# Kernel tuning notes

Hardware: AMD Instinct MI355X
Metric: run time of the kernel (lower is better)

## Reference

```python
import jax, jax.numpy as jnp
import numpy as np

N = 10000      # nodes
E = 100000     # edges
C = 32         # in_channels == hidden_channels == out_channels
ED = 4         # edge_dim
G = 64         # number of graphs in the batch
EPS = 1e-5     # BatchNorm eps


def setup_inputs() -> dict:
    key = jax.random.key(0)
    ks = jax.random.split(key, 20)
    rn = lambda k, shape, s=0.05: jax.random.normal(k, shape, dtype=jnp.float32) * s
    return {
        "x": jax.random.normal(ks[0], (N, C), dtype=jnp.float32),
        "edge_attr": jax.random.normal(ks[1], (E, ED), dtype=jnp.float32),
        # edge MLP 1: ED -> C -> C*C ; NNConv1 root/bias
        "e1_w1": rn(ks[2], (ED, C)), "e1_b1": jnp.zeros((C,), jnp.float32),
        "e1_w2": rn(ks[3], (C, C * C)), "e1_b2": jnp.zeros((C * C,), jnp.float32),
        "root1": rn(ks[4], (C, C)), "bias1": jnp.zeros((C,), jnp.float32),
        # edge MLP 2: ED -> C -> C*C ; NNConv2 root/bias
        "e2_w1": rn(ks[5], (ED, C)), "e2_b1": jnp.zeros((C,), jnp.float32),
        "e2_w2": rn(ks[6], (C, C * C)), "e2_b2": jnp.zeros((C * C,), jnp.float32),
        "root2": rn(ks[7], (C, C)), "bias2": jnp.zeros((C,), jnp.float32),
        # BatchNorm (eval mode: running stats)
        "bn1_g": jnp.ones((C,), jnp.float32), "bn1_b": jnp.zeros((C,), jnp.float32),
        "bn1_m": rn(ks[8], (C,), 0.1), "bn1_v": 1.0 + 0.1 * jax.random.uniform(ks[9], (C,), dtype=jnp.float32),
        "bn2_g": jnp.ones((C,), jnp.float32), "bn2_b": jnp.zeros((C,), jnp.float32),
        "bn2_m": rn(ks[10], (C,), 0.1), "bn2_v": 1.0 + 0.1 * jax.random.uniform(ks[11], (C,), dtype=jnp.float32),
        # readout: C -> C//2 -> 1
        "r1_w": rn(ks[12], (C, C // 2)), "r1_b": jnp.zeros((C // 2,), jnp.float32),
        "r2_w": rn(ks[13], (C // 2, 1)), "r2_b": jnp.zeros((1,), jnp.float32),
        "edge_index": jax.random.randint(ks[14], (2, E), 0, N),
        "batch": jnp.sort(jax.random.randint(ks[15], (N,), 0, G)),
    }


def _nnconv(x, edge_index, edge_attr, w1, b1, w2, b2, root, bias):
    # edge MLP -> per-edge weight matrix [E, C, C]
    h = jax.nn.relu(edge_attr @ w1 + b1)
    W = (h @ w2 + b2).reshape(E, C, C)
    src, dst = edge_index[0], edge_index[1]
    # gather source features, per-edge matmul, scatter-mean to target nodes
    msg = jnp.einsum('ei,eio->eo', x[src], W)                      # [E, C]
    agg = jax.ops.segment_sum(msg, dst, num_segments=N)            # [N, C]
    cnt = jax.ops.segment_sum(jnp.ones((E,), x.dtype), dst, num_segments=N)
    agg = agg / jnp.maximum(cnt, 1.0)[:, None]
    return agg + x @ root + bias


def _bn(x, g, b, m, v):
    return (x - m) * jax.lax.rsqrt(v + EPS) * g + b


def reference(x, edge_attr,
              e1_w1, e1_b1, e1_w2, e1_b2, root1, bias1,
              e2_w1, e2_b1, e2_w2, e2_b2, root2, bias2,
              bn1_g, bn1_b, bn1_m, bn1_v,
              bn2_g, bn2_b, bn2_m, bn2_v,
              r1_w, r1_b, r2_w, r2_b,
              edge_index, batch):
    h = jax.nn.relu(_bn(_nnconv(x, edge_index, edge_attr, e1_w1, e1_b1, e1_w2, e1_b2, root1, bias1),
                        bn1_g, bn1_b, bn1_m, bn1_v))
    h = jax.nn.relu(_bn(_nnconv(h, edge_index, edge_attr, e2_w1, e2_b1, e2_w2, e2_b2, root2, bias2),
                        bn2_g, bn2_b, bn2_m, bn2_v))
    # global mean pool over graphs
    psum = jax.ops.segment_sum(h, batch, num_segments=G)           # [G, C]
    pcnt = jax.ops.segment_sum(jnp.ones((N,), h.dtype), batch, num_segments=G)
    pooled = psum / jnp.maximum(pcnt, 1.0)[:, None]
    # readout MLP (dropout is identity in eval)
    return jax.nn.relu(pooled @ r1_w + r1_b) @ r2_w + r2_b          # [G, 1]
```

## Files before the change

kernel.cpp:

```cpp
#include <hip/hip_runtime.h>

#define NN 10000
#define EE 100000
#define CC 32
#define GG 64
#define EPSV 1e-5f
#define NB 8
#define SLOTS 1056
#define HST 36
#define PST 36
#define PNODE (32*PST)
#define EBLK (EE/8)
#define WBLK 160

__global__ __launch_bounds__(256) void k_init(const float* __restrict__ edge_attr,
        const float* __restrict__ w1a, const float* __restrict__ b1a,
        const float* __restrict__ w1b, const float* __restrict__ b1b,
        const int* __restrict__ ei,
        float* __restrict__ hbuf1, float* __restrict__ hbuf2,
        int* __restrict__ cnt, int* __restrict__ deg,
        const float* __restrict__ w2a, const float* __restrict__ b2a,
        const float* __restrict__ w2b, const float* __restrict__ b2b,
        float* __restrict__ w2r1, float* __restrict__ w2r2) {
    int blk = blockIdx.x;
    int t = threadIdx.x;
    if (blk < EBLK) {
        int e = blk * 8 + (t >> 5);
        int o = t & 31;
        float4 a = *(const float4*)&edge_attr[(size_t)e * 4];
        float ha = fmaxf(a.x * w1a[o] + a.y * w1a[32 + o] + a.z * w1a[64 + o] + a.w * w1a[96 + o] + b1a[o], 0.f);
        float hb = fmaxf(a.x * w1b[o] + a.y * w1b[32 + o] + a.z * w1b[64 + o] + a.w * w1b[96 + o] + b1b[o], 0.f);
        hbuf1[(size_t)e * HST + o] = ha;
        hbuf2[(size_t)e * HST + o] = hb;
        if (o < 4) {
            float pad = (o == 0) ? 1.f : 0.f;
            hbuf1[(size_t)e * HST + 32 + o] = pad;
            hbuf2[(size_t)e * HST + 32 + o] = pad;
        }
        if (o == 0) {
            atomicAdd(&cnt[ei[EE + e]], 1);
            atomicAdd(&deg[ei[e]], 1);
        }
    } else {
        int b2i = blk - EBLK;
        int s = (b2i % 5) * 256 + t;
        int i = b2i / 5;
        if (s < SLOTS) {
            float va = (s < 1024) ? w2a[(s >> 5) * 1024 + i * 32 + (s & 31)]
                                  : b2a[i * 32 + (s - 1024)];
            float vb = (s < 1024) ? w2b[(s >> 5) * 1024 + i * 32 + (s & 31)]
                                  : b2b[i * 32 + (s - 1024)];
            w2r1[i * SLOTS + s] = va;
            w2r2[i * SLOTS + s] = vb;
        }
    }
}

__global__ __launch_bounds__(1024) void k_scan(const int* __restrict__ deg,
                                               int* __restrict__ rowptr,
                                               int* __restrict__ cursor) {
    __shared__ int buf[1024];
    int t = threadIdx.x;
    int v[10]; int s = 0;
    int base = t * 10;
    #pragma unroll
    for (int k = 0; k < 10; k++) {
        int idx = base + k;
        v[k] = (idx < NN) ? deg[idx] : 0;
        s += v[k];
    }
    buf[t] = s;
    for (int off = 1; off < 1024; off <<= 1) {
        __syncthreads();
        int val = buf[t] + ((t >= off) ? buf[t - off] : 0);
        __syncthreads();
        buf[t] = val;
    }
    __syncthreads();
    int carry = (t > 0) ? buf[t - 1] : 0;
    #pragma unroll
    for (int k = 0; k < 10; k++) {
        int idx = base + k;
        if (idx < NN) { rowptr[idx] = carry; cursor[idx] = carry; }
        carry += v[k];
    }
    if (t == 1023) rowptr[NN] = buf[1023];
}

__global__ void k_scatter(const int* __restrict__ ei,
                          int* __restrict__ cursor, int* __restrict__ csr_eid) {
    int e = blockIdx.x * blockDim.x + threadIdx.x;
    if (e >= EE) return;
    int pos = atomicAdd(&cursor[ei[e]], 1);
    csr_eid[pos] = e;
}

__global__ __launch_bounds__(256, 3) void k_fused3(const float* __restrict__ x,
        const float* __restrict__ hbuf,
        const float* __restrict__ w2r,
        const int* __restrict__ ei, const int* __restrict__ rowptr,
        const int* __restrict__ csr_eid, float* __restrict__ agg) {
    __shared__ float xs[NB][32];
    __shared__ float P2[NB * PNODE];
    int t = threadIdx.x;
    int o = t & 31;
    int cb = 4 * (t >> 5);
    int n0 = blockIdx.x * NB;

    xs[t >> 5][t & 31] = x[n0 * 32 + t];
    __syncthreads();

    {
        float acc[4][NB];
        #pragma unroll
        for (int k = 0; k < 4; k++)
            #pragma unroll
            for (int n = 0; n < NB; n++) acc[k][n] = 0.f;
        #pragma unroll
        for (int j = 0; j < 8; j++) {
            float wk[4][4];
            #pragma unroll
            for (int r = 0; r < 4; r++)
                #pragma unroll
                for (int k = 0; k < 4; k++)
                    wk[r][k] = w2r[(4 * j + r) * SLOTS + (cb + k) * 32 + o];
            #pragma unroll
            for (int n = 0; n < NB; n++) {
                float4 xq = *(const float4*)&xs[n][4 * j];
                #pragma unroll
                for (int k = 0; k < 4; k++)
                    acc[k][n] += xq.x * wk[0][k] + xq.y * wk[1][k]
                               + xq.z * wk[2][k] + xq.w * wk[3][k];
            }
        }
        #pragma unroll
        for (int n = 0; n < NB; n++) {
            float4 st = make_float4(acc[0][n], acc[1][n], acc[2][n], acc[3][n]);
            *(float4*)&P2[n * PNODE + o * PST + cb] = st;
        }
    }
    if (t < 32) {
        float wb[32];
        #pragma unroll
        for (int i = 0; i < 32; i++) wb[i] = w2r[i * SLOTS + 1024 + t];
        #pragma unroll
        for (int n = 0; n < NB; n++) {
            float b = 0.f;
            #pragma unroll
            for (int j = 0; j < 8; j++) {
                float4 xq = *(const float4*)&xs[n][4 * j];
                b += xq.x * wb[4 * j] + xq.y * wb[4 * j + 1]
                   + xq.z * wb[4 * j + 2] + xq.w * wb[4 * j + 3];
            }
            *(float4*)&P2[n * PNODE + t * PST + 32] = make_float4(b, 0.f, 0.f, 0.f);
        }
    }
    __syncthreads();

    int ebase = rowptr[n0];
    int eend  = rowptr[n0 + NB];
    int grp = t >> 5;
    int pos = ebase + grp;
    int e_c = 0, src_c = 0, dst_c = 0;
    float4 hq[9];
    if (pos < eend) {
        e_c = csr_eid[pos];
        src_c = ei[e_c];
        dst_c = ei[EE + e_c];
        const float* hb = &hbuf[(size_t)e_c * HST];
        #pragma unroll
        for (int b = 0; b < 9; b++) hq[b] = *(const float4*)&hb[4 * b];
    }
    while (pos < eend) {
        int pos_n = pos + 8;
        int e_n = 0, src_n = 0, dst_n = 0;
        float4 hq_n[9];
        if (pos_n < eend) {
            e_n = csr_eid[pos_n];
            src_n = ei[e_n];
            dst_n = ei[EE + e_n];
            const float* hbn = &hbuf[(size_t)e_n * HST];
            #pragma unroll
            for (int b = 0; b < 9; b++) hq_n[b] = *(const float4*)&hbn[4 * b];
        }
        const float* Pn = &P2[(src_c - n0) * PNODE + o * PST];
        float msg = 0.f;
        #pragma unroll
        for (int b = 0; b < 9; b++) {
            float4 pq = *(const float4*)&Pn[4 * b];
            msg += hq[b].x * pq.x + hq[b].y * pq.y
                 + hq[b].z * pq.z + hq[b].w * pq.w;
        }
        atomicAdd(&agg[(size_t)dst_c * 32 + o], msg);
        pos = pos_n; e_c = e_n; src_c = src_n; dst_c = dst_n;
        #pragma unroll
        for (int b = 0; b < 9; b++) hq[b] = hq_n[b];
    }
}

__global__ __launch_bounds__(256) void k_combine(const float* __restrict__ x_in,
        float* __restrict__ agg, const int* __restrict__ cnt,
        const float* __restrict__ root, const float* __restrict__ bias,
        const float* __restrict__ bng, const float* __restrict__ bnb,
        const float* __restrict__ bnm, const float* __restrict__ bnv,
        float* __restrict__ x_out, float* __restrict__ psum,
        const int* __restrict__ batch) {
    __shared__ float xs[8][32];
    __shared__ float vals[8][32];
    __shared__ int gb[8];
    int t = threadIdx.x;
    int n0 = blockIdx.x * 8;
    xs[t >> 5][t & 31] = x_in[n0 * 32 + t];
    __syncthreads();
    int k = t >> 5, o = t & 31, n = n0 + k;
    float r = bias[o];
    #pragma unroll
    for (int i = 0; i < 32; i++) r += xs[k][i] * root[i * 32 + o];
    float a = agg[(size_t)n * 32 + o] / fmaxf((float)cnt[n], 1.f);
    float val = a + r;
    val = (val - bnm[o]) * rsqrtf(bnv[o] + EPSV) * bng[o] + bnb[o];
    val = fmaxf(val, 0.f);
    if (x_out) {
        x_out[(size_t)n * 32 + o] = val;
        agg[(size_t)n * 32 + o] = 0.f;
    }
    if (psum) {
        vals[k][o] = val;
        if (o == 0) gb[k] = batch[n];
        __syncthreads();
        if (k == 0) {
            float acc = vals[0][o];
            int g = gb[0];
            #pragma unroll
            for (int k2 = 1; k2 < 8; k2++) {
                if (gb[k2] == g) acc += vals[k2][o];
                else {
                    atomicAdd(&psum[(size_t)g * 32 + o], acc);
                    g = gb[k2]; acc = vals[k2][o];
                }
            }
            atomicAdd(&psum[(size_t)g * 32 + o], acc);
        }
    }
}

__global__ __launch_bounds__(256) void k_readout(const float* __restrict__ psum,
        const int* __restrict__ batch,
        const float* __restrict__ r1w, const float* __restrict__ r1b,
        const float* __restrict__ r2w, const float* __restrict__ r2b,
        float* __restrict__ out) {
    __shared__ float w1s[32 * 16];
    __shared__ float b1s[16];
    __shared__ float w2s[16];
    __shared__ float ps[GG * 32];
    int t = threadIdx.x;
    int cnt_g = 0;
    if (t < GG) {
        int lo = 0, hi = NN;
        while (lo < hi) { int m = (lo + hi) >> 1; if (batch[m] < t) lo = m + 1; else hi = m; }
        int lb = lo;
        lo = 0; hi = NN;
        while (lo < hi) { int m = (lo + hi) >> 1; if (batch[m] < t + 1) lo = m + 1; else hi = m; }
        cnt_g = lo - lb;
    }
    w1s[t] = r1w[t];
    w1s[t + 256] = r1w[t + 256];
    if (t < 16) { b1s[t] = r1b[t]; w2s[t] = r2w[t]; }
    #pragma unroll
    for (int i = 0; i < GG * 32 / 256; i++) ps[t + i * 256] = psum[t + i * 256];
    __syncthreads();
    if (t < GG) {
        float inv = 1.f / fmaxf((float)cnt_g, 1.f);
        float acc = r2b[0];
        #pragma unroll
        for (int j = 0; j < 16; j++) {
            float dot = 0.f;
            #pragma unroll
            for (int c = 0; c < 32; c++) dot += ps[t * 32 + c] * w1s[c * 16 + j];
            float z = dot * inv + b1s[j];
            acc += fmaxf(z, 0.f) * w2s[j];
        }
        out[t] = acc;
    }
}

extern "C" void kernel_launch(void* const* d_in, const int* in_sizes, int n_in,
                              void* d_out, int out_size, void* d_ws, size_t ws_size,
                              hipStream_t stream) {
    const float* x       = (const float*)d_in[0];
    const float* eattr   = (const float*)d_in[1];
    const float* e1_w1   = (const float*)d_in[2];
    const float* e1_b1   = (const float*)d_in[3];
    const float* e1_w2   = (const float*)d_in[4];
    const float* e1_b2   = (const float*)d_in[5];
    const float* root1   = (const float*)d_in[6];
    const float* bias1   = (const float*)d_in[7];
    const float* e2_w1   = (const float*)d_in[8];
    const float* e2_b1   = (const float*)d_in[9];
    const float* e2_w2   = (const float*)d_in[10];
    const float* e2_b2   = (const float*)d_in[11];
    const float* root2   = (const float*)d_in[12];
    const float* bias2   = (const float*)d_in[13];
    const float* bn1_g   = (const float*)d_in[14];
    const float* bn1_b   = (const float*)d_in[15];
    const float* bn1_m   = (const float*)d_in[16];
    const float* bn1_v   = (const float*)d_in[17];
    const float* bn2_g   = (const float*)d_in[18];
    const float* bn2_b   = (const float*)d_in[19];
    const float* bn2_m   = (const float*)d_in[20];
    const float* bn2_v   = (const float*)d_in[21];
    const float* r1_w    = (const float*)d_in[22];
    const float* r1_b    = (const float*)d_in[23];
    const float* r2_w    = (const float*)d_in[24];
    const float* r2_b    = (const float*)d_in[25];
    const int*   ei      = (const int*)d_in[26];
    const int*   batch   = (const int*)d_in[27];

    char* ws = (char*)d_ws;
    float* hbuf1  = (float*)(ws);
    float* hbuf2  = (float*)(ws + 14400000);
    float* w2r1   = (float*)(ws + 28800000);
    float* w2r2   = (float*)(ws + 28935168);
    float* agg    = (float*)(ws + 29070336);
    int*   cnt    = (int*)  (ws + 30350336);
    int*   deg    = (int*)  (ws + 30390336);
    float* psum   = (float*)(ws + 30430336);
    float* xmid   = (float*)(ws + 30438528);
    int*   rowptr = (int*)  (ws + 31718528);
    int*   cursor = (int*)  (ws + 31758592);
    int*   csr    = (int*)  (ws + 31798592);

    hipMemsetAsync(ws + 29070336, 0, 1368192, stream);

    k_init<<<EBLK + WBLK, 256, 0, stream>>>(eattr, e1_w1, e1_b1, e2_w1, e2_b1, ei,
                                            hbuf1, hbuf2, cnt, deg,
                                            e1_w2, e1_b2, e2_w2, e2_b2, w2r1, w2r2);
    k_scan<<<1, 1024, 0, stream>>>(deg, rowptr, cursor);
    k_scatter<<<(EE + 255) / 256, 256, 0, stream>>>(ei, cursor, csr);

    k_fused3<<<NN / NB, 256, 0, stream>>>(x, hbuf1, w2r1, ei, rowptr, csr, agg);
    k_combine<<<NN / 8, 256, 0, stream>>>(x, agg, cnt, root1, bias1,
                                          bn1_g, bn1_b, bn1_m, bn1_v,
                                          xmid, nullptr, batch);

    k_fused3<<<NN / NB, 256, 0, stream>>>(xmid, hbuf2, w2r2, ei, rowptr, csr, agg);
    k_combine<<<NN / 8, 256, 0, stream>>>(xmid, agg, cnt, root2, bias2,
                                          bn2_g, bn2_b, bn2_m, bn2_v,
                                          nullptr, psum, batch);

    k_readout<<<1, 256, 0, stream>>>(psum, batch, r1_w, r1_b, r2_w, r2_b, (float*)d_out);
}
```

Before: 248.7 us.

## Store edge hidden features in CSR order and pack src/dst metadata

Edge hidden activations are now computed in a separate kernel after the CSR build and written in CSR position order. The aggregation kernel can then read them contiguously by position instead of through a gather by edge id. Source and destination indices are packed into an int2 array during scatter, which removes the indirect csr_eid->ei loads. The padded bias lane is dropped (HST 36->32), and the bias term is read directly from P2. The cost is an extra kernel launch and an extra indirect read of edge_attr, placed before the two aggregation passes.

```diff
diff --git a/kernel.cpp b/kernel.cpp
--- a/kernel.cpp
+++ b/kernel.cpp
@@ -7,42 +7,28 @@
 #define EPSV 1e-5f
 #define NB 8
 #define SLOTS 1056
-#define HST 36
+#define HST 32
 #define PST 36
 #define PNODE (32*PST)
 #define EBLK (EE/8)
+#define HBLK ((EE+255)/256)
 #define WBLK 160
 
-__global__ __launch_bounds__(256) void k_init(const float* __restrict__ edge_attr,
-        const float* __restrict__ w1a, const float* __restrict__ b1a,
-        const float* __restrict__ w1b, const float* __restrict__ b1b,
-        const int* __restrict__ ei,
-        float* __restrict__ hbuf1, float* __restrict__ hbuf2,
+__global__ __launch_bounds__(256) void k_pre(const int* __restrict__ ei,
         int* __restrict__ cnt, int* __restrict__ deg,
         const float* __restrict__ w2a, const float* __restrict__ b2a,
         const float* __restrict__ w2b, const float* __restrict__ b2b,
         float* __restrict__ w2r1, float* __restrict__ w2r2) {
     int blk = blockIdx.x;
     int t = threadIdx.x;
-    if (blk < EBLK) {
-        int e = blk * 8 + (t >> 5);
-        int o = t & 31;
-        float4 a = *(const float4*)&edge_attr[(size_t)e * 4];
-        float ha = fmaxf(a.x * w1a[o] + a.y * w1a[32 + o] + a.z * w1a[64 + o] + a.w * w1a[96 + o] + b1a[o], 0.f);
-        float hb = fmaxf(a.x * w1b[o] + a.y * w1b[32 + o] + a.z * w1b[64 + o] + a.w * w1b[96 + o] + b1b[o], 0.f);
-        hbuf1[(size_t)e * HST + o] = ha;
-        hbuf2[(size_t)e * HST + o] = hb;
-        if (o < 4) {
-            float pad = (o == 0) ? 1.f : 0.f;
-            hbuf1[(size_t)e * HST + 32 + o] = pad;
-            hbuf2[(size_t)e * HST + 32 + o] = pad;
-        }
-        if (o == 0) {
+    if (blk < HBLK) {
+        int e = blk * 256 + t;
+        if (e < EE) {
             atomicAdd(&cnt[ei[EE + e]], 1);
             atomicAdd(&deg[ei[e]], 1);
         }
     } else {
-        int b2i = blk - EBLK;
+        int b2i = blk - HBLK;
         int s = (b2i % 5) * 256 + t;
         int i = b2i / 5;
         if (s < SLOTS) {
@@ -88,18 +74,38 @@
 }
 
 __global__ void k_scatter(const int* __restrict__ ei,
-                          int* __restrict__ cursor, int* __restrict__ csr_eid) {
+                          int* __restrict__ cursor, int* __restrict__ csr_eid,
+                          int2* __restrict__ meta) {
     int e = blockIdx.x * blockDim.x + threadIdx.x;
     if (e >= EE) return;
-    int pos = atomicAdd(&cursor[ei[e]], 1);
+    int s = ei[e];
+    int d = ei[EE + e];
+    int pos = atomicAdd(&cursor[s], 1);
     csr_eid[pos] = e;
+    meta[pos] = make_int2(s, d);
+}
+
+__global__ __launch_bounds__(256) void k_h(const float* __restrict__ edge_attr,
+        const float* __restrict__ w1a, const float* __restrict__ b1a,
+        const float* __restrict__ w1b, const float* __restrict__ b1b,
+        const int* __restrict__ csr_eid,
+        float* __restrict__ hbuf1, float* __restrict__ hbuf2) {
+    int t = threadIdx.x;
+    int pos = blockIdx.x * 8 + (t >> 5);
+    int o = t & 31;
+    int e = csr_eid[pos];
+    float4 a = *(const float4*)&edge_attr[(size_t)e * 4];
+    float ha = fmaxf(a.x * w1a[o] + a.y * w1a[32 + o] + a.z * w1a[64 + o] + a.w * w1a[96 + o] + b1a[o], 0.f);
+    float hb = fmaxf(a.x * w1b[o] + a.y * w1b[32 + o] + a.z * w1b[64 + o] + a.w * w1b[96 + o] + b1b[o], 0.f);
+    hbuf1[(size_t)pos * HST + o] = ha;
+    hbuf2[(size_t)pos * HST + o] = hb;
 }
 
 __global__ __launch_bounds__(256, 3) void k_fused3(const float* __restrict__ x,
         const float* __restrict__ hbuf,
         const float* __restrict__ w2r,
-        const int* __restrict__ ei, const int* __restrict__ rowptr,
-        const int* __restrict__ csr_eid, float* __restrict__ agg) {
+        const int2* __restrict__ meta, const int* __restrict__ rowptr,
+        float* __restrict__ agg) {
     __shared__ float xs[NB][32];
     __shared__ float P2[NB * PNODE];
     int t = threadIdx.x;
@@ -161,40 +167,38 @@
     int eend  = rowptr[n0 + NB];
     int grp = t >> 5;
     int pos = ebase + grp;
-    int e_c = 0, src_c = 0, dst_c = 0;
-    float4 hq[9];
+    int src_c = 0, dst_c = 0;
+    float4 hq[8];
     if (pos < eend) {
-        e_c = csr_eid[pos];
-        src_c = ei[e_c];
-        dst_c = ei[EE + e_c];
-        const float* hb = &hbuf[(size_t)e_c * HST];
-        #pragma unroll
-        for (int b = 0; b < 9; b++) hq[b] = *(const float4*)&hb[4 * b];
+        int2 sd = meta[pos];
+        src_c = sd.x; dst_c = sd.y;
+        const float* hb = &hbuf[(size_t)pos * HST];
+        #pragma unroll
+        for (int b = 0; b < 8; b++) hq[b] = *(const float4*)&hb[4 * b];
     }
     while (pos < eend) {
         int pos_n = pos + 8;
-        int e_n = 0, src_n = 0, dst_n = 0;
-        float4 hq_n[9];
+        int src_n = 0, dst_n = 0;
+        float4 hq_n[8];
         if (pos_n < eend) {
-            e_n = csr_eid[pos_n];
-            src_n = ei[e_n];
-            dst_n = ei[EE + e_n];
-            const float* hbn = &hbuf[(size_t)e_n * HST];
-            #pragma unroll
-            for (int b = 0; b < 9; b++) hq_n[b] = *(const float4*)&hbn[4 * b];
+            int2 sd = meta[pos_n];
+            src_n = sd.x; dst_n = sd.y;
+            const float* hbn = &hbuf[(size_t)pos_n * HST];
+            #pragma unroll
+            for (int b = 0; b < 8; b++) hq_n[b] = *(const float4*)&hbn[4 * b];
         }
         const float* Pn = &P2[(src_c - n0) * PNODE + o * PST];
-        float msg = 0.f;
-        #pragma unroll
-        for (int b = 0; b < 9; b++) {
+        float msg = Pn[32];
+        #pragma unroll
+        for (int b = 0; b < 8; b++) {
             float4 pq = *(const float4*)&Pn[4 * b];
             msg += hq[b].x * pq.x + hq[b].y * pq.y
                  + hq[b].z * pq.z + hq[b].w * pq.w;
         }
         atomicAdd(&agg[(size_t)dst_c * 32 + o], msg);
-        pos = pos_n; e_c = e_n; src_c = src_n; dst_c = dst_n;
-        #pragma unroll
-        for (int b = 0; b < 9; b++) hq[b] = hq_n[b];
+        pos = pos_n; src_c = src_n; dst_c = dst_n;
+        #pragma unroll
+        for (int b = 0; b < 8; b++) hq[b] = hq_n[b];
     }
 }
 
@@ -318,32 +322,33 @@
 
     char* ws = (char*)d_ws;
     float* hbuf1  = (float*)(ws);
-    float* hbuf2  = (float*)(ws + 14400000);
-    float* w2r1   = (float*)(ws + 28800000);
-    float* w2r2   = (float*)(ws + 28935168);
-    float* agg    = (float*)(ws + 29070336);
-    int*   cnt    = (int*)  (ws + 30350336);
-    int*   deg    = (int*)  (ws + 30390336);
-    float* psum   = (float*)(ws + 30430336);
-    float* xmid   = (float*)(ws + 30438528);
-    int*   rowptr = (int*)  (ws + 31718528);
-    int*   cursor = (int*)  (ws + 31758592);
-    int*   csr    = (int*)  (ws + 31798592);
-
-    hipMemsetAsync(ws + 29070336, 0, 1368192, stream);
-
-    k_init<<<EBLK + WBLK, 256, 0, stream>>>(eattr, e1_w1, e1_b1, e2_w1, e2_b1, ei,
-                                            hbuf1, hbuf2, cnt, deg,
-                                            e1_w2, e1_b2, e2_w2, e2_b2, w2r1, w2r2);
+    float* hbuf2  = (float*)(ws + 12800000);
+    float* w2r1   = (float*)(ws + 25600000);
+    float* w2r2   = (float*)(ws + 25735168);
+    float* agg    = (float*)(ws + 25870336);
+    int*   cnt    = (int*)  (ws + 27150336);
+    int*   deg    = (int*)  (ws + 27190336);
+    float* psum   = (float*)(ws + 27230336);
+    float* xmid   = (float*)(ws + 27238528);
+    int*   rowptr = (int*)  (ws + 28518528);
+    int*   cursor = (int*)  (ws + 28558592);
+    int*   csr    = (int*)  (ws + 28598592);
+    int2*  meta   = (int2*) (ws + 28998592);
+
+    hipMemsetAsync(ws + 25870336, 0, 1368192, stream);
+
+    k_pre<<<HBLK + WBLK, 256, 0, stream>>>(ei, cnt, deg,
+                                           e1_w2, e1_b2, e2_w2, e2_b2, w2r1, w2r2);
     k_scan<<<1, 1024, 0, stream>>>(deg, rowptr, cursor);
-    k_scatter<<<(EE + 255) / 256, 256, 0, stream>>>(ei, cursor, csr);
-
-    k_fused3<<<NN / NB, 256, 0, stream>>>(x, hbuf1, w2r1, ei, rowptr, csr, agg);
+    k_scatter<<<(EE + 255) / 256, 256, 0, stream>>>(ei, cursor, csr, meta);
+    k_h<<<EBLK, 256, 0, stream>>>(eattr, e1_w1, e1_b1, e2_w1, e2_b1, csr, hbuf1, hbuf2);
+
+    k_fused3<<<NN / NB, 256, 0, stream>>>(x, hbuf1, w2r1, meta, rowptr, agg);
     k_combine<<<NN / 8, 256, 0, stream>>>(x, agg, cnt, root1, bias1,
                                           bn1_g, bn1_b, bn1_m, bn1_v,
                                           xmid, nullptr, batch);
 
-    k_fused3<<<NN / NB, 256, 0, stream>>>(xmid, hbuf2, w2r2, ei, rowptr, csr, agg);
+    k_fused3<<<NN / NB, 256, 0, stream>>>(xmid, hbuf2, w2r2, meta, rowptr, agg);
     k_combine<<<NN / 8, 256, 0, stream>>>(xmid, agg, cnt, root2, bias2,
                                           bn2_g, bn2_b, bn2_m, bn2_v,
                                           nullptr, psum, batch);
```

New measurement: 242.0 us. 2.7% less time.
